# Kernel optimization log

Hardware: AMD Instinct MI355X
Metric: run time of the kernel (lower is better)

The kernel has to match this reference:

```python
import jax, jax.numpy as jnp
import numpy as np

HID = 128          # hidden_dim
IN_DIM = 256       # input_dim
BOT = 128          # bottleneck_dim
OUT = 4            # output_dim
NQ = 131072        # num query (mesh) points
E = 262144         # num grid->query edges
SEQ = 262144       # grid points (64^3)
B = 1
PE_DIM = 4 * HID   # 512, sincos embed dim over ndim=4


def _linear_params(key, fin, fout):
    k1, k2 = jax.random.split(key)
    lim = 1.0 / np.sqrt(fin)
    w = jax.random.uniform(k1, (fin, fout), minval=-lim, maxval=lim, dtype=jnp.float32)
    b = jax.random.uniform(k2, (fout,), minval=-lim, maxval=lim, dtype=jnp.float32)
    return w, b


def setup_inputs() -> dict:
    key = jax.random.key(0)
    ks = jax.random.split(key, 10)
    x = jax.random.normal(ks[0], (B, SEQ, IN_DIM), dtype=jnp.float32)
    # raw positions in [0, 200) so query_pos/100 - 1 lands in [-1, 1)
    query_pos = jax.random.uniform(ks[1], (NQ, 3), dtype=jnp.float32) * 200.0
    qidx = jnp.sort(jax.random.randint(ks[2], (E,), 0, NQ))          # sorted, as segment_csr assumes
    gidx = jax.random.randint(ks[3], (E,), 0, B * SEQ)
    grid_to_query_edges = jnp.stack([qidx, gidx], axis=1)            # [E, 2] (query_idx, grid_idx)

    msg_w0, msg_b0 = _linear_params(ks[4], IN_DIM + PE_DIM, 512)
    msg_w1, msg_b1 = _linear_params(ks[5], 512, 256)
    msg_w2, msg_b2 = _linear_params(ks[6], 256, BOT)
    pred_w0, pred_b0 = _linear_params(ks[7], BOT, 256)
    pred_w1, pred_b1 = _linear_params(ks[8], 256, OUT)
    return dict(x=x, query_pos=query_pos, grid_to_query_edges=grid_to_query_edges,
                msg_w0=msg_w0, msg_b0=msg_b0, msg_w1=msg_w1, msg_b1=msg_b1,
                msg_w2=msg_w2, msg_b2=msg_b2,
                pred_w0=pred_w0, pred_b0=pred_b0, pred_w1=pred_w1, pred_b1=pred_b1)


def _sincos_embed(coords):
    # coords: [N, 4]; dim=512 -> 128 per coord -> 64 frequencies (no padding needed)
    eff = PE_DIM // 4
    omega = 1.0 / (10000.0 ** (jnp.arange(0, eff, 2, dtype=jnp.float32) / eff))  # [64]
    out = coords[..., None] * omega                                  # [N, 4, 64]
    emb = jnp.concatenate([jnp.sin(out), jnp.cos(out)], axis=-1)     # [N, 4, 128]
    return emb.reshape(coords.shape[0], -1)                          # [N, 512]


def _gelu(x):
    return jax.nn.gelu(x, approximate=False)  # torch nn.GELU default is exact erf


def reference(x, query_pos, grid_to_query_edges,
              msg_w0, msg_b0, msg_w1, msg_b1, msg_w2, msg_b2,
              pred_w0, pred_b0, pred_w1, pred_b1):
    qp = query_pos / 100.0 - 1.0
    ones = jnp.ones((qp.shape[0], 1), dtype=qp.dtype)
    qp = jnp.concatenate([qp, ones], axis=1)                         # [NQ, 4]
    pe = _sincos_embed(qp)                                           # [NQ, 512]

    xf = x.reshape(-1, x.shape[-1])                                  # [B*SEQ, IN_DIM]
    qidx = grid_to_query_edges[:, 0]
    gidx = grid_to_query_edges[:, 1]

    feat = jnp.concatenate([xf[gidx], pe[qidx]], axis=1)             # [E, 768]
    h = _gelu(feat @ msg_w0 + msg_b0)
    h = _gelu(h @ msg_w1 + msg_b1)
    h = h @ msg_w2 + msg_b2                                          # [E, BOT]

    nq = qp.shape[0]
    sums = jax.ops.segment_sum(h, qidx, num_segments=nq)             # [NQ, BOT]
    counts = jax.ops.segment_sum(jnp.ones((h.shape[0],), h.dtype), qidx, num_segments=nq)
    mean = sums / jnp.maximum(counts, 1.0)[:, None]                  # empty segments -> 0 (segment_csr mean)

    out = _gelu(mean @ pred_w0 + pred_b0) @ pred_w1 + pred_b1        # [NQ, OUT]
    return out
```

## Files before the change

kernel.cpp:

```cpp
#include <hip/hip_runtime.h>
#include <cmath>

#define IN_DIM   256
#define H0_DIM   512
#define H1_DIM   256
#define BOT      128
#define NQ_      131072
#define NE_      262144
#define SEQ_     262144
#define QWIN     32768
#define NWIN     (NQ_/QWIN)
#define PE_K     384

static const size_t OFF_XH    = 0;
static const size_t OFF_XL    = 134217728;
static const size_t OFF_Z     = 268435456;
static const size_t OFF_PEH   = 536870912;
static const size_t OFF_PEL   = 562036736;
static const size_t OFF_H2    = 738197504;
static const size_t OFF_W0AH  = 872415232;
static const size_t OFF_W0AL  = 872677376;
static const size_t OFF_W0BH  = 872939520;
static const size_t OFF_W0BL  = 873332736;
static const size_t OFF_W1H   = 873725952;
static const size_t OFF_W1L   = 873988096;
static const size_t OFF_W2H   = 874250240;
static const size_t OFF_W2L   = 874315776;
static const size_t OFF_PW0H  = 874381312;
static const size_t OFF_PW0L  = 874446848;
static const size_t OFF_BCONST= 874512384;
static const size_t OFF_START = 874514432;
static const size_t OFF_MEANH = 0;
static const size_t OFF_MEANL = 33554432;
static const size_t OFF_G1    = 268435456;

typedef __attribute__((ext_vector_type(8))) short bf16x8;
typedef __attribute__((ext_vector_type(4))) float f32x4;

__device__ __forceinline__ float gelu_f(float v) {
    return v * 0.5f * (1.0f + erff(v * 0.7071067811865476f));
}
__device__ __forceinline__ unsigned short f2bf(float f) {
    unsigned int u = __float_as_uint(f);
    unsigned int r = (u + 0x7FFFu + ((u >> 16) & 1u)) >> 16;
    return (unsigned short)r;
}
__device__ __forceinline__ float bf2f(unsigned short h) {
    return __uint_as_float(((unsigned int)h) << 16);
}
__device__ __forceinline__ unsigned int pack2(unsigned short a, unsigned short b) {
    return (unsigned int)a | ((unsigned int)b << 16);
}
__device__ __forceinline__ void stage16(const void* g, void* l) {
    __builtin_amdgcn_global_load_lds(
        (const __attribute__((address_space(1))) unsigned int*)g,
        (__attribute__((address_space(3))) unsigned int*)l,
        16, 0, 0);
}
__device__ __forceinline__ void cvt4(const float4 v, unsigned int* hw, unsigned int* lw) {
    const unsigned short a = f2bf(v.x), b = f2bf(v.y), c = f2bf(v.z), d = f2bf(v.w);
    hw[0] = pack2(a, b); hw[1] = pack2(c, d);
    lw[0] = pack2(f2bf(v.x - bf2f(a)), f2bf(v.y - bf2f(b)));
    lw[1] = pack2(f2bf(v.z - bf2f(c)), f2bf(v.w - bf2f(d)));
}

__global__ __launch_bounds__(256) void conv_x(
    const float* __restrict__ x,
    unsigned short* __restrict__ xH, unsigned short* __restrict__ xL)
{
    const int wv = threadIdx.x >> 6;
    const int l  = threadIdx.x & 63;
    const int row = blockIdx.x * 4 + wv;
    const size_t base = (size_t)row * IN_DIM + l * 4;
    float4 v = *(const float4*)&x[base];
    unsigned short h0 = f2bf(v.x), h1 = f2bf(v.y), h2 = f2bf(v.z), h3 = f2bf(v.w);
    uint2 H, L;
    H.x = pack2(h0, h1); H.y = pack2(h2, h3);
    L.x = pack2(f2bf(v.x - bf2f(h0)), f2bf(v.y - bf2f(h1)));
    L.y = pack2(f2bf(v.z - bf2f(h2)), f2bf(v.w - bf2f(h3)));
    *(uint2*)&xH[base] = H;
    *(uint2*)&xL[base] = L;
}

__global__ __launch_bounds__(256) void conv_w(
    const float* __restrict__ W, unsigned short* __restrict__ WTh,
    unsigned short* __restrict__ WTl, int K, int N)
{
    int idx = blockIdx.x * 256 + threadIdx.x;
    if (idx >= K * N) return;
    int k = idx / N, n = idx % N;
    float v = W[idx];
    unsigned short h = f2bf(v);
    WTh[(size_t)n * K + k] = h;
    WTl[(size_t)n * K + k] = f2bf(v - bf2f(h));
}

__global__ __launch_bounds__(256) void bias_fold(
    const float* __restrict__ w0, const float* __restrict__ b0,
    float* __restrict__ bconst)
{
    int n = blockIdx.x * 256 + threadIdx.x;
    if (n >= H0_DIM) return;
    float s = b0[n];
    for (int j = 0; j < 64; ++j) {
        float om = exp2f((float)j * (-13.287712379549449f / 64.0f));
        s += sinf(om) * w0[(size_t)(640 + j) * H0_DIM + n];
        s += cosf(om) * w0[(size_t)(704 + j) * H0_DIM + n];
    }
    bconst[n] = s;
}

__global__ __launch_bounds__(256) void seg_offsets(
    const int* __restrict__ edges, int* __restrict__ start)
{
    int e = blockIdx.x * 256 + threadIdx.x;
    if (e > NE_) return;
    int qc = (e < NE_) ? edges[2 * e] : NQ_;
    int qp = (e > 0) ? edges[2 * e - 2] : -1;
    for (int q = qp + 1; q <= qc; ++q) start[q] = e;
}

__global__ __launch_bounds__(256) void build_pe(
    const float* __restrict__ qpos, int qbase,
    unsigned short* __restrict__ peH, unsigned short* __restrict__ peL)
{
    const int wv = threadIdx.x >> 6;
    const int l  = threadIdx.x & 63;
    const int i  = blockIdx.x * 4 + wv;
    const int i0 = l * 8;
    if (i0 >= PE_K) return;
    const int q  = qbase + i;
    const size_t base = (size_t)i * PE_K;

    const int cc = i0 >> 7;
    const int j0 = i0 & 127;
    const float cv = qpos[q * 3 + cc] * 0.01f - 1.0f;
    const bool is_sin = (j0 < 64);
    const int jj0 = j0 & 63;
    unsigned int hw[4], lw[4];
    #pragma unroll
    for (int p2 = 0; p2 < 4; ++p2) {
        unsigned short hh[2], ll[2];
        #pragma unroll
        for (int s = 0; s < 2; ++s) {
            int jj = jj0 + p2 * 2 + s;
            float om  = exp2f((float)jj * (-13.287712379549449f / 64.0f));
            float arg = cv * om;
            float v   = is_sin ? __sinf(arg) : __cosf(arg);
            unsigned short h = f2bf(v);
            hh[s] = h; ll[s] = f2bf(v - bf2f(h));
        }
        hw[p2] = pack2(hh[0], hh[1]);
        lw[p2] = pack2(ll[0], ll[1]);
    }
    uint4 H, L;
    H.x = hw[0]; H.y = hw[1]; H.z = hw[2]; H.w = hw[3];
    L.x = lw[0]; L.y = lw[1]; L.z = lw[2]; L.w = lw[3];
    *(uint4*)&peH[base + i0] = H;
    *(uint4*)&peL[base + i0] = L;
}

template <int ACT, int OUT_MODE, int GATHER>
__global__ __launch_bounds__(256) void gemm_mfma(
    const unsigned short* __restrict__ Ah, const unsigned short* __restrict__ Al,
    const unsigned short* __restrict__ Bh, const unsigned short* __restrict__ Bl,
    const float* __restrict__ bias,
    float* __restrict__ Cf, unsigned short* __restrict__ ChO, unsigned short* __restrict__ ClO,
    int M, int K, int N,
    const int* __restrict__ gp, const float* __restrict__ Zw)
{
    __shared__ __align__(16) short lds[4][128][32];

    const int tid = threadIdx.x;
    const int w   = tid >> 6;
    const int l   = tid & 63;
    const int l16 = l & 15;
    const int lq  = l >> 4;
    const int bm  = blockIdx.y * 128;
    const int bn  = blockIdx.x * 128;
    const int wm  = (w & 1) * 64;
    const int wn  = (w >> 1) * 64;

    f32x4 acc[4][4];
    #pragma unroll
    for (int i = 0; i < 4; ++i)
        #pragma unroll
        for (int j = 0; j < 4; ++j)
            acc[i][j] = (f32x4){0.f, 0.f, 0.f, 0.f};

    const int jrow = l >> 2;
    const int jkc  = l & 3;
    const int t0 = w * 2, t1 = t0 + 1;
    const int r0 = t0 * 16 + jrow, r1 = t1 * 16 + jrow;

    size_t arow0, arow1;
    if (GATHER) {
        arow0 = (size_t)gp[2 * (bm + r0) + 1] * K;
        arow1 = (size_t)gp[2 * (bm + r1) + 1] * K;
    } else {
        arow0 = (size_t)(bm + r0) * K;
        arow1 = (size_t)(bm + r1) * K;
    }
    const size_t brow0 = (size_t)(bn + r0) * K;
    const size_t brow1 = (size_t)(bn + r1) * K;
    short* d00 = &lds[0][0][0] + t0 * 512;
    short* d01 = &lds[1][0][0] + t0 * 512;
    short* d02 = &lds[2][0][0] + t0 * 512;
    short* d03 = &lds[3][0][0] + t0 * 512;
    short* d10 = &lds[0][0][0] + t1 * 512;
    short* d11 = &lds[1][0][0] + t1 * 512;
    short* d12 = &lds[2][0][0] + t1 * 512;
    short* d13 = &lds[3][0][0] + t1 * 512;

    for (int k0 = 0; k0 < K; k0 += 32) {
        const int ko = k0 + jkc * 8;
        stage16(Ah + arow0 + ko, d00);
        stage16(Al + arow0 + ko, d01);
        stage16(Bh + brow0 + ko, d02);
        stage16(Bl + brow0 + ko, d03);
        stage16(Ah + arow1 + ko, d10);
        stage16(Al + arow1 + ko, d11);
        stage16(Bh + brow1 + ko, d12);
        stage16(Bl + brow1 + ko, d13);
        __syncthreads();

        bf16x8 ah[4], al[4], bh[4], bl[4];
        #pragma unroll
        for (int i = 0; i < 4; ++i) {
            ah[i] = *(const bf16x8*)&lds[0][wm + i*16 + l16][lq*8];
            al[i] = *(const bf16x8*)&lds[1][wm + i*16 + l16][lq*8];
            bh[i] = *(const bf16x8*)&lds[2][wn + i*16 + l16][lq*8];
            bl[i] = *(const bf16x8*)&lds[3][wn + i*16 + l16][lq*8];
        }
        #pragma unroll
        for (int i = 0; i < 4; ++i)
            #pragma unroll
            for (int j = 0; j < 4; ++j) {
                acc[i][j] = __builtin_amdgcn_mfma_f32_16x16x32_bf16(ah[i], bh[j], acc[i][j], 0, 0, 0);
                acc[i][j] = __builtin_amdgcn_mfma_f32_16x16x32_bf16(ah[i], bl[j], acc[i][j], 0, 0, 0);
                acc[i][j] = __builtin_amdgcn_mfma_f32_16x16x32_bf16(al[i], bh[j], acc[i][j], 0, 0, 0);
            }
        __syncthreads();
    }

    if (OUT_MODE == 0) {
        #pragma unroll
        for (int j = 0; j < 4; ++j) {
            int n = bn + wn + j * 16 + l16;
            float bv = bias[n];
            #pragma unroll
            for (int i = 0; i < 4; ++i) {
                int mrow = bm + wm + i * 16 + lq * 4;
                #pragma unroll
                for (int r = 0; r < 4; ++r) {
                    float v = acc[i][j][r] + bv;
                    if (ACT) v = gelu_f(v);
                    Cf[(size_t)(mrow + r) * N + n] = v;
                }
            }
        }
    } else if (OUT_MODE == 1) {
        float* lbuf = ((float*)&lds[0][0][0]) + w * 2048;
        #pragma unroll
        for (int h = 0; h < 2; ++h) {
            #pragma unroll
            for (int j2 = 0; j2 < 2; ++j2) {
                int j = 2 * h + j2;
                float bv = bias[bn + wn + j * 16 + l16];
                #pragma unroll
                for (int i = 0; i < 4; ++i) {
                    #pragma unroll
                    for (int r = 0; r < 4; ++r) {
                        int rowq = i * 16 + lq * 4 + r;
                        int col  = j2 * 16 + l16;
                        float v = acc[i][j][r] + bv;
                        if (ACT) v = gelu_f(v);
                        lbuf[rowq * 32 + (((col >> 2) ^ (rowq & 7)) << 2) + (col & 3)] = v;
                    }
                }
            }
            __syncthreads();
            {
                const size_t grow = (size_t)(bm + wm + l);
                unsigned short* ph = ChO + grow * N + bn + wn + h * 32;
                unsigned short* pl = ClO + grow * N + bn + wn + h * 32;
                #pragma unroll
                for (int cc = 0; cc < 4; ++cc) {
                    unsigned int hw[4], lw[4];
                    #pragma unroll
                    for (int c2 = 0; c2 < 2; ++c2) {
                        int cq = cc * 2 + c2;
                        float4 v = *(const float4*)&lbuf[l * 32 + ((cq ^ (l & 7)) << 2)];
                        unsigned short ha = f2bf(v.x), hb = f2bf(v.y);
                        unsigned short hc = f2bf(v.z), hd = f2bf(v.w);
                        hw[c2*2+0] = pack2(ha, hb);
                        hw[c2*2+1] = pack2(hc, hd);
                        lw[c2*2+0] = pack2(f2bf(v.x - bf2f(ha)), f2bf(v.y - bf2f(hb)));
                        lw[c2*2+1] = pack2(f2bf(v.z - bf2f(hc)), f2bf(v.w - bf2f(hd)));
                    }
                    uint4 H, L;
                    H.x = hw[0]; H.y = hw[1]; H.z = hw[2]; H.w = hw[3];
                    L.x = lw[0]; L.y = lw[1]; L.z = lw[2]; L.w = lw[3];
                    *(uint4*)&ph[cc * 8] = H;
                    *(uint4*)&pl[cc * 8] = L;
                }
            }
            __syncthreads();
        }
    } else {
        const int q = gp[2 * (bm + wm + l)];
        float* lbuf = ((float*)&lds[0][0][0]) + w * 2048;
        #pragma unroll
        for (int h = 0; h < 2; ++h) {
            #pragma unroll
            for (int j2 = 0; j2 < 2; ++j2) {
                int j = 2 * h + j2;
                #pragma unroll
                for (int i = 0; i < 4; ++i) {
                    #pragma unroll
                    for (int r = 0; r < 4; ++r) {
                        int rowq = i * 16 + lq * 4 + r;
                        int col  = j2 * 16 + l16;
                        lbuf[rowq * 32 + (((col >> 2) ^ (rowq & 7)) << 2) + (col & 3)] = acc[i][j][r];
                    }
                }
            }
            __syncthreads();
            {
                const size_t grow = (size_t)(bm + wm + l);
                const float* zrow = Zw + (size_t)q * H0_DIM + bn + wn + h * 32;
                unsigned short* ph = ChO + grow * N + bn + wn + h * 32;
                unsigned short* pl = ClO + grow * N + bn + wn + h * 32;
                #pragma unroll
                for (int cc = 0; cc < 4; ++cc) {
                    unsigned int hw[4], lw[4];
                    #pragma unroll
                    for (int c2 = 0; c2 < 2; ++c2) {
                        int cq = cc * 2 + c2;
                        float4 v = *(const float4*)&lbuf[l * 32 + ((cq ^ (l & 7)) << 2)];
                        float4 z = *(const float4*)&zrow[cq * 4];
                        v.x = gelu_f(v.x + z.x); v.y = gelu_f(v.y + z.y);
                        v.z = gelu_f(v.z + z.z); v.w = gelu_f(v.w + z.w);
                        unsigned short ha = f2bf(v.x), hb = f2bf(v.y);
                        unsigned short hc = f2bf(v.z), hd = f2bf(v.w);
                        hw[c2*2+0] = pack2(ha, hb);
                        hw[c2*2+1] = pack2(hc, hd);
                        lw[c2*2+0] = pack2(f2bf(v.x - bf2f(ha)), f2bf(v.y - bf2f(hb)));
                        lw[c2*2+1] = pack2(f2bf(v.z - bf2f(hc)), f2bf(v.w - bf2f(hd)));
                    }
                    uint4 H, L;
                    H.x = hw[0]; H.y = hw[1]; H.z = hw[2]; H.w = hw[3];
                    L.x = lw[0]; L.y = lw[1]; L.z = lw[2]; L.w = lw[3];
                    *(uint4*)&ph[cc * 8] = H;
                    *(uint4*)&pl[cc * 8] = L;
                }
            }
            __syncthreads();
        }
    }
}

__global__ __launch_bounds__(512, 2) void fused_edge(
    const unsigned short* __restrict__ xHg, const unsigned short* __restrict__ xLg,
    const unsigned short* __restrict__ w0aHg, const unsigned short* __restrict__ w0aLg,
    const unsigned short* __restrict__ w1Hg, const unsigned short* __restrict__ w1Lg,
    const unsigned short* __restrict__ w2Hg, const unsigned short* __restrict__ w2Lg,
    const float* __restrict__ Zg, const float* __restrict__ b1g,
    const float* __restrict__ b2g, const int* __restrict__ gp,
    float* __restrict__ h2g)
{
    extern __shared__ __align__(16) short smem[];
    short* stg = smem;
    short* h0h = smem + 16384;
    short* h0l = smem + 32768;

    const int tid = threadIdx.x;
    const int w   = tid >> 6;
    const int l   = tid & 63;
    const int l16 = l & 15;
    const int lq  = l >> 4;
    const int bm  = blockIdx.x * 128;

    const int wm  = (w & 1) * 64;
    const int wn  = (w >> 1) * 32;
    const int wn1 = (w >> 1) * 64;

    const int srow  = l >> 2;
    const int sunit = l & 3;
    const int r_s   = w * 16 + srow;
    const size_t a_off = (size_t)gp[2 * (bm + r_s) + 1] * IN_DIM + sunit * 8;
    const int q_e = gp[2 * (bm + wm + l)];
    float* lbuf = ((float*)smem) + w * 1024;

    f32x4 h1acc[4][4];
    #pragma unroll
    for (int i = 0; i < 4; ++i)
        #pragma unroll
        for (int j = 0; j < 4; ++j)
            h1acc[i][j] = (f32x4){0.f, 0.f, 0.f, 0.f};

    for (int c = 0; c < 4; ++c) {
        const size_t b0_off = (size_t)(c * 128 + r_s) * IN_DIM + sunit * 8;
        f32x4 acc1[4][2];
        #pragma unroll
        for (int i = 0; i < 4; ++i)
            #pragma unroll
            for (int j = 0; j < 2; ++j)
                acc1[i][j] = (f32x4){0.f, 0.f, 0.f, 0.f};

        stage16(xHg + a_off,    stg + w * 512);
        stage16(xLg + a_off,    stg + 4096 + w * 512);
        stage16(w0aHg + b0_off, stg + 8192 + w * 512);
        stage16(w0aLg + b0_off, stg + 12288 + w * 512);
        __syncthreads();
        for (int ks = 0; ks < 8; ++ks) {
            bf16x8 ah[4], al[4], bh[2], bl[2];
            #pragma unroll
            for (int i = 0; i < 4; ++i) {
                const int ro = (wm + i * 16 + l16) * 32 + lq * 8;
                ah[i] = *(const bf16x8*)&stg[ro];
                al[i] = *(const bf16x8*)&stg[4096 + ro];
            }
            #pragma unroll
            for (int j = 0; j < 2; ++j) {
                const int ro = (wn + j * 16 + l16) * 32 + lq * 8;
                bh[j] = *(const bf16x8*)&stg[8192 + ro];
                bl[j] = *(const bf16x8*)&stg[12288 + ro];
            }
            __syncthreads();
            if (ks < 7) {
                const int k0n = (ks + 1) * 32;
                stage16(xHg + a_off + k0n,    stg + w * 512);
                stage16(xLg + a_off + k0n,    stg + 4096 + w * 512);
                stage16(w0aHg + b0_off + k0n, stg + 8192 + w * 512);
                stage16(w0aLg + b0_off + k0n, stg + 12288 + w * 512);
            }
            #pragma unroll
            for (int i = 0; i < 4; ++i)
                #pragma unroll
                for (int j = 0; j < 2; ++j) {
                    acc1[i][j] = __builtin_amdgcn_mfma_f32_16x16x32_bf16(ah[i], bh[j], acc1[i][j], 0, 0, 0);
                    acc1[i][j] = __builtin_amdgcn_mfma_f32_16x16x32_bf16(ah[i], bl[j], acc1[i][j], 0, 0, 0);
                    acc1[i][j] = __builtin_amdgcn_mfma_f32_16x16x32_bf16(al[i], bh[j], acc1[i][j], 0, 0, 0);
                }
            __syncthreads();
        }

        #pragma unroll
        for (int hh = 0; hh < 2; ++hh) {
            #pragma unroll
            for (int i = 0; i < 4; ++i)
                #pragma unroll
                for (int r = 0; r < 4; ++r) {
                    const int rowq = i * 16 + lq * 4 + r;
                    lbuf[rowq * 16 + ((((l16 >> 2) ^ (rowq & 3)) << 2) | (l16 & 3))] = acc1[i][hh][r];
                }
            __syncthreads();
            {
                const int row = wm + l;
                const float* zrow = Zg + (size_t)q_e * H0_DIM + c * 128 + wn + hh * 16;
                unsigned int hw[8], lw[8];
                #pragma unroll
                for (int cq = 0; cq < 4; ++cq) {
                    float4 v = *(const float4*)&lbuf[l * 16 + ((cq ^ (l & 3)) << 2)];
                    const float4 z = *(const float4*)&zrow[cq * 4];
                    v.x = gelu_f(v.x + z.x); v.y = gelu_f(v.y + z.y);
                    v.z = gelu_f(v.z + z.z); v.w = gelu_f(v.w + z.w);
                    cvt4(v, &hw[cq * 2], &lw[cq * 2]);
                }
                const int u0 = (wn + hh * 16) >> 3;
                const int o0 = row * 128 + (((u0    ) ^ (row & 7)) << 3);
                const int o1 = row * 128 + (((u0 + 1) ^ (row & 7)) << 3);
                uint4 H0, H1, L0, L1;
                H0.x = hw[0]; H0.y = hw[1]; H0.z = hw[2]; H0.w = hw[3];
                H1.x = hw[4]; H1.y = hw[5]; H1.z = hw[6]; H1.w = hw[7];
                L0.x = lw[0]; L0.y = lw[1]; L0.z = lw[2]; L0.w = lw[3];
                L1.x = lw[4]; L1.y = lw[5]; L1.z = lw[6]; L1.w = lw[7];
                *(uint4*)&h0h[o0] = H0; *(uint4*)&h0h[o1] = H1;
                *(uint4*)&h0l[o0] = L0; *(uint4*)&h0l[o1] = L1;
            }
            __syncthreads();
        }

        {
            const size_t r0 = (size_t)(w * 32 + srow) * H0_DIM + c * 128 + sunit * 8;
            stage16(w1Hg + r0,               stg + w * 1024);
            stage16(w1Hg + r0 + 16 * H0_DIM, stg + w * 1024 + 512);
            stage16(w1Lg + r0,               stg + 8192 + w * 1024);
            stage16(w1Lg + r0 + 16 * H0_DIM, stg + 8192 + w * 1024 + 512);
        }
        __syncthreads();
        for (int ks = 0; ks < 4; ++ks) {
            bf16x8 ah[4], al[4], bh[4], bl[4];
            #pragma unroll
            for (int i = 0; i < 4; ++i) {
                const int row = wm + i * 16 + l16;
                const int uo = (((ks * 4 + lq) ^ (row & 7)) << 3);
                ah[i] = *(const bf16x8*)&h0h[row * 128 + uo];
                al[i] = *(const bf16x8*)&h0l[row * 128 + uo];
            }
            #pragma unroll
            for (int j = 0; j < 4; ++j) {
                const int ro = (wn1 + j * 16 + l16) * 32 + lq * 8;
                bh[j] = *(const bf16x8*)&stg[ro];
                bl[j] = *(const bf16x8*)&stg[8192 + ro];
            }
            __syncthreads();
            if (ks < 3) {
                const size_t r0 = (size_t)(w * 32 + srow) * H0_DIM + c * 128 + (ks + 1) * 32 + sunit * 8;
                stage16(w1Hg + r0,               stg + w * 1024);
                stage16(w1Hg + r0 + 16 * H0_DIM, stg + w * 1024 + 512);
                stage16(w1Lg + r0,               stg + 8192 + w * 1024);
                stage16(w1Lg + r0 + 16 * H0_DIM, stg + 8192 + w * 1024 + 512);
            }
            #pragma unroll
            for (int i = 0; i < 4; ++i)
                #pragma unroll
                for (int j = 0; j < 4; ++j) {
                    h1acc[i][j] = __builtin_amdgcn_mfma_f32_16x16x32_bf16(ah[i], bh[j], h1acc[i][j], 0, 0, 0);
                    h1acc[i][j] = __builtin_amdgcn_mfma_f32_16x16x32_bf16(ah[i], bl[j], h1acc[i][j], 0, 0, 0);
                    h1acc[i][j] = __builtin_amdgcn_mfma_f32_16x16x32_bf16(al[i], bh[j], h1acc[i][j], 0, 0, 0);
                }
            __syncthreads();
        }
    }

    f32x4 acc2[4][2];
    #pragma unroll
    for (int i = 0; i < 4; ++i)
        #pragma unroll
        for (int j = 0; j < 2; ++j)
            acc2[i][j] = (f32x4){0.f, 0.f, 0.f, 0.f};
    const int mykh = w >> 2;

    for (int kh = 0; kh < 2; ++kh) {
        #pragma unroll
        for (int hh = 0; hh < 4; ++hh) {
            if (mykh == kh) {
                const float bv = b1g[wn1 + hh * 16 + l16];
                #pragma unroll
                for (int i = 0; i < 4; ++i)
                    #pragma unroll
                    for (int r = 0; r < 4; ++r) {
                        const int rowq = i * 16 + lq * 4 + r;
                        lbuf[rowq * 16 + ((((l16 >> 2) ^ (rowq & 3)) << 2) | (l16 & 3))] =
                            gelu_f(h1acc[i][hh][r] + bv);
                    }
            }
            __syncthreads();
            if (mykh == kh) {
                const int row = wm + l;
                unsigned int hw[8], lw[8];
                #pragma unroll
                for (int cq = 0; cq < 4; ++cq) {
                    float4 v = *(const float4*)&lbuf[l * 16 + ((cq ^ (l & 3)) << 2)];
                    cvt4(v, &hw[cq * 2], &lw[cq * 2]);
                }
                const int u0 = ((wn1 & 127) + hh * 16) >> 3;
                const int o0 = row * 128 + (((u0    ) ^ (row & 7)) << 3);
                const int o1 = row * 128 + (((u0 + 1) ^ (row & 7)) << 3);
                uint4 H0, H1, L0, L1;
                H0.x = hw[0]; H0.y = hw[1]; H0.z = hw[2]; H0.w = hw[3];
                H1.x = hw[4]; H1.y = hw[5]; H1.z = hw[6]; H1.w = hw[7];
                L0.x = lw[0]; L0.y = lw[1]; L0.z = lw[2]; L0.w = lw[3];
                L1.x = lw[4]; L1.y = lw[5]; L1.z = lw[6]; L1.w = lw[7];
                *(uint4*)&h0h[o0] = H0; *(uint4*)&h0h[o1] = H1;
                *(uint4*)&h0l[o0] = L0; *(uint4*)&h0l[o1] = L1;
            }
            __syncthreads();
        }

        {
            const unsigned short* Wsrc = (w < 4) ? w2Hg : w2Lg;
            const size_t r0 = (size_t)((w & 3) * 32 + srow) * H1_DIM + kh * 128 + sunit * 8;
            short* dst = stg + (w >> 2) * 4096 + (w & 3) * 1024;
            stage16(Wsrc + r0,               dst);
            stage16(Wsrc + r0 + 16 * H1_DIM, dst + 512);
        }
        __syncthreads();
        for (int ks = 0; ks < 4; ++ks) {
            bf16x8 ah[4], al[4], bh[2], bl[2];
            #pragma unroll
            for (int i = 0; i < 4; ++i) {
                const int row = wm + i * 16 + l16;
                const int uo = (((ks * 4 + lq) ^ (row & 7)) << 3);
                ah[i] = *(const bf16x8*)&h0h[row * 128 + uo];
                al[i] = *(const bf16x8*)&h0l[row * 128 + uo];
            }
            #pragma unroll
            for (int j = 0; j < 2; ++j) {
                const int ro = (wn + j * 16 + l16) * 32 + lq * 8;
                bh[j] = *(const bf16x8*)&stg[ro];
                bl[j] = *(const bf16x8*)&stg[4096 + ro];
            }
            __syncthreads();
            if (ks < 3) {
                const unsigned short* Wsrc = (w < 4) ? w2Hg : w2Lg;
                const size_t r0 = (size_t)((w & 3) * 32 + srow) * H1_DIM + kh * 128 + (ks + 1) * 32 + sunit * 8;
                short* dst = stg + (w >> 2) * 4096 + (w & 3) * 1024;
                stage16(Wsrc + r0,               dst);
                stage16(Wsrc + r0 + 16 * H1_DIM, dst + 512);
            }
            #pragma unroll
            for (int i = 0; i < 4; ++i)
                #pragma unroll
                for (int j = 0; j < 2; ++j) {
                    acc2[i][j] = __builtin_amdgcn_mfma_f32_16x16x32_bf16(ah[i], bh[j], acc2[i][j], 0, 0, 0);
                    acc2[i][j] = __builtin_amdgcn_mfma_f32_16x16x32_bf16(ah[i], bl[j], acc2[i][j], 0, 0, 0);
                    acc2[i][j] = __builtin_amdgcn_mfma_f32_16x16x32_bf16(al[i], bh[j], acc2[i][j], 0, 0, 0);
                }
            __syncthreads();
        }
    }

    #pragma unroll
    for (int j = 0; j < 2; ++j) {
        const int n = wn + j * 16 + l16;
        const float bv = b2g[n];
        #pragma unroll
        for (int i = 0; i < 4; ++i) {
            const int er = bm + wm + i * 16 + lq * 4;
            #pragma unroll
            for (int r = 0; r < 4; ++r)
                h2g[(size_t)(er + r) * BOT + n] = acc2[i][j][r] + bv;
        }
    }
}

__global__ __launch_bounds__(256) void seg_mean(
    const int* __restrict__ start, const float* __restrict__ h2,
    unsigned short* __restrict__ mH, unsigned short* __restrict__ mL)
{
    const int t = threadIdx.x;
    const int q = blockIdx.x * 8 + (t >> 5);
    const int quad = t & 31;
    const int s = start[q];
    const int e = start[q + 1];

    float4 acc = make_float4(0.f, 0.f, 0.f, 0.f);
    for (int i = s; i < e; ++i) {
        const float4 v = *(const float4*)&h2[(size_t)i * BOT + quad * 4];
        acc.x += v.x; acc.y += v.y; acc.z += v.z; acc.w += v.w;
    }
    const float inv = 1.0f / (float)((e - s) > 0 ? (e - s) : 1);
    float m0 = acc.x * inv, m1 = acc.y * inv, m2 = acc.z * inv, m3 = acc.w * inv;
    unsigned short h0 = f2bf(m0), h1 = f2bf(m1), h2s = f2bf(m2), h3 = f2bf(m3);
    uint2 H, L;
    H.x = pack2(h0, h1); H.y = pack2(h2s, h3);
    L.x = pack2(f2bf(m0 - bf2f(h0)), f2bf(m1 - bf2f(h1)));
    L.y = pack2(f2bf(m2 - bf2f(h2s)), f2bf(m3 - bf2f(h3)));
    *(uint2*)&mH[(size_t)q * BOT + quad * 4] = H;
    *(uint2*)&mL[(size_t)q * BOT + quad * 4] = L;
}

__global__ __launch_bounds__(256) void pred1_kernel(
    const float* __restrict__ g1, const float* __restrict__ w,
    const float* __restrict__ b, float* __restrict__ out)
{
    const int wave = threadIdx.x >> 6;
    const int lane = threadIdx.x & 63;
    const int row  = blockIdx.x * 4 + wave;

    const float* g = g1 + (size_t)row * 256;
    float a0 = 0, a1 = 0, a2 = 0, a3 = 0;
    #pragma unroll
    for (int i = 0; i < 4; ++i) {
        int k = lane + 64 * i;
        float gv = g[k];
        const float* wr = w + k * 4;
        a0 = fmaf(gv, wr[0], a0);
        a1 = fmaf(gv, wr[1], a1);
        a2 = fmaf(gv, wr[2], a2);
        a3 = fmaf(gv, wr[3], a3);
    }
    #pragma unroll
    for (int off = 32; off > 0; off >>= 1) {
        a0 += __shfl_down(a0, off, 64);
        a1 += __shfl_down(a1, off, 64);
        a2 += __shfl_down(a2, off, 64);
        a3 += __shfl_down(a3, off, 64);
    }
    if (lane == 0) {
        float4 o = {a0 + b[0], a1 + b[1], a2 + b[2], a3 + b[3]};
        *(float4*)&out[(size_t)row * 4] = o;
    }
}

extern "C" void kernel_launch(void* const* d_in, const int* in_sizes, int n_in,
                              void* d_out, int out_size, void* d_ws, size_t ws_size,
                              hipStream_t stream)
{
    const float* x    = (const float*)d_in[0];
    const float* qpos = (const float*)d_in[1];
    const int*   edges= (const int*)  d_in[2];
    const float* w0   = (const float*)d_in[3];
    const float* b0   = (const float*)d_in[4];
    const float* w1   = (const float*)d_in[5];
    const float* b1   = (const float*)d_in[6];
    const float* w2   = (const float*)d_in[7];
    const float* b2   = (const float*)d_in[8];
    const float* pw0  = (const float*)d_in[9];
    const float* pb0  = (const float*)d_in[10];
    const float* pw1  = (const float*)d_in[11];
    const float* pb1  = (const float*)d_in[12];
    float* out = (float*)d_out;

    char* ws = (char*)d_ws;
    unsigned short* xH    = (unsigned short*)(ws + OFF_XH);
    unsigned short* xL    = (unsigned short*)(ws + OFF_XL);
    float*          Z     = (float*)(ws + OFF_Z);
    unsigned short* peH   = (unsigned short*)(ws + OFF_PEH);
    unsigned short* peL   = (unsigned short*)(ws + OFF_PEL);
    float*          h2    = (float*)(ws + OFF_H2);
    unsigned short* w0aH  = (unsigned short*)(ws + OFF_W0AH);
    unsigned short* w0aL  = (unsigned short*)(ws + OFF_W0AL);
    unsigned short* w0bH  = (unsigned short*)(ws + OFF_W0BH);
    unsigned short* w0bL  = (unsigned short*)(ws + OFF_W0BL);
    unsigned short* w1H   = (unsigned short*)(ws + OFF_W1H);
    unsigned short* w1L   = (unsigned short*)(ws + OFF_W1L);
    unsigned short* w2H   = (unsigned short*)(ws + OFF_W2H);
    unsigned short* w2L   = (unsigned short*)(ws + OFF_W2L);
    unsigned short* pw0H  = (unsigned short*)(ws + OFF_PW0H);
    unsigned short* pw0L  = (unsigned short*)(ws + OFF_PW0L);
    float*          bconst= (float*)(ws + OFF_BCONST);
    int*            start = (int*)(ws + OFF_START);
    unsigned short* meanH = (unsigned short*)(ws + OFF_MEANH);
    unsigned short* meanL = (unsigned short*)(ws + OFF_MEANL);
    float*          g1    = (float*)(ws + OFF_G1);

    static bool attr_done = false;
    if (!attr_done) {
        hipFuncSetAttribute(reinterpret_cast<const void*>(&fused_edge),
                            hipFuncAttributeMaxDynamicSharedMemorySize, 98304);
        attr_done = true;
    }

    conv_x<<<SEQ_/4, 256, 0, stream>>>(x, xH, xL);
    conv_w<<<(IN_DIM*H0_DIM + 255)/256, 256, 0, stream>>>(w0, w0aH, w0aL, IN_DIM, H0_DIM);
    conv_w<<<(PE_K*H0_DIM + 255)/256, 256, 0, stream>>>(w0 + (size_t)IN_DIM*H0_DIM, w0bH, w0bL, PE_K, H0_DIM);
    conv_w<<<(H0_DIM*H1_DIM + 255)/256, 256, 0, stream>>>(w1, w1H, w1L, H0_DIM, H1_DIM);
    conv_w<<<(H1_DIM*BOT + 255)/256, 256, 0, stream>>>(w2, w2H, w2L, H1_DIM, BOT);
    conv_w<<<(BOT*H1_DIM + 255)/256, 256, 0, stream>>>(pw0, pw0H, pw0L, BOT, H1_DIM);
    bias_fold<<<2, 256, 0, stream>>>(w0, b0, bconst);
    seg_offsets<<<(NE_ + 1 + 255)/256, 256, 0, stream>>>(edges, start);

    for (int wn = 0; wn < NWIN; ++wn) {
        build_pe<<<QWIN/4, 256, 0, stream>>>(qpos, wn * QWIN, peH, peL);
        gemm_mfma<0, 0, 0><<<dim3(H0_DIM/128, QWIN/128), 256, 0, stream>>>(
            peH, peL, w0bH, w0bL, bconst, Z + (size_t)wn * QWIN * H0_DIM,
            nullptr, nullptr, QWIN, PE_K, H0_DIM, nullptr, nullptr);
    }

    fused_edge<<<NE_/128, 512, 98304, stream>>>(
        xH, xL, w0aH, w0aL, w1H, w1L, w2H, w2L,
        Z, b1, b2, edges, h2);

    seg_mean<<<NQ_/8, 256, 0, stream>>>(start, h2, meanH, meanL);
    gemm_mfma<1, 0, 0><<<dim3(H1_DIM/128, NQ_/128), 256, 0, stream>>>(
        meanH, meanL, pw0H, pw0L, pb0, g1, nullptr, nullptr,
        NQ_, BOT, H1_DIM, nullptr, nullptr);
    pred1_kernel<<<NQ_/4, 256, 0, stream>>>(g1, pw1, pb1, out);
}
```

Before: 1.672 ms.

## Shrink fused edge kernel tile to 64 edges with 4 warps

The fused edge MLP kernel now processes 64 edges per block with 256 threads instead of 128 edges with 512 threads. Every warp covers all 64 rows and takes a distinct column slice, so all staging, epilogue and LDS layouts are rewritten and dynamic shared memory drops from 96KB to 64KB. The aim is higher occupancy and more blocks in flight, paying for it with more weight staging per edge, since each weight tile is now reused across only 64 rows. The unused OUT_MODE 1/2 epilogues of the generic GEMM are also deleted.

```diff
diff --git a/kernel.cpp b/kernel.cpp
--- a/kernel.cpp
+++ b/kernel.cpp
@@ -259,108 +259,10 @@
                 }
             }
         }
-    } else if (OUT_MODE == 1) {
-        float* lbuf = ((float*)&lds[0][0][0]) + w * 2048;
-        #pragma unroll
-        for (int h = 0; h < 2; ++h) {
-            #pragma unroll
-            for (int j2 = 0; j2 < 2; ++j2) {
-                int j = 2 * h + j2;
-                float bv = bias[bn + wn + j * 16 + l16];
-                #pragma unroll
-                for (int i = 0; i < 4; ++i) {
-                    #pragma unroll
-                    for (int r = 0; r < 4; ++r) {
-                        int rowq = i * 16 + lq * 4 + r;
-                        int col  = j2 * 16 + l16;
-                        float v = acc[i][j][r] + bv;
-                        if (ACT) v = gelu_f(v);
-                        lbuf[rowq * 32 + (((col >> 2) ^ (rowq & 7)) << 2) + (col & 3)] = v;
-                    }
-                }
-            }
-            __syncthreads();
-            {
-                const size_t grow = (size_t)(bm + wm + l);
-                unsigned short* ph = ChO + grow * N + bn + wn + h * 32;
-                unsigned short* pl = ClO + grow * N + bn + wn + h * 32;
-                #pragma unroll
-                for (int cc = 0; cc < 4; ++cc) {
-                    unsigned int hw[4], lw[4];
-                    #pragma unroll
-                    for (int c2 = 0; c2 < 2; ++c2) {
-                        int cq = cc * 2 + c2;
-                        float4 v = *(const float4*)&lbuf[l * 32 + ((cq ^ (l & 7)) << 2)];
-                        unsigned short ha = f2bf(v.x), hb = f2bf(v.y);
-                        unsigned short hc = f2bf(v.z), hd = f2bf(v.w);
-                        hw[c2*2+0] = pack2(ha, hb);
-                        hw[c2*2+1] = pack2(hc, hd);
-                        lw[c2*2+0] = pack2(f2bf(v.x - bf2f(ha)), f2bf(v.y - bf2f(hb)));
-                        lw[c2*2+1] = pack2(f2bf(v.z - bf2f(hc)), f2bf(v.w - bf2f(hd)));
-                    }
-                    uint4 H, L;
-                    H.x = hw[0]; H.y = hw[1]; H.z = hw[2]; H.w = hw[3];
-                    L.x = lw[0]; L.y = lw[1]; L.z = lw[2]; L.w = lw[3];
-                    *(uint4*)&ph[cc * 8] = H;
-                    *(uint4*)&pl[cc * 8] = L;
-                }
-            }
-            __syncthreads();
-        }
-    } else {
-        const int q = gp[2 * (bm + wm + l)];
-        float* lbuf = ((float*)&lds[0][0][0]) + w * 2048;
-        #pragma unroll
-        for (int h = 0; h < 2; ++h) {
-            #pragma unroll
-            for (int j2 = 0; j2 < 2; ++j2) {
-                int j = 2 * h + j2;
-                #pragma unroll
-                for (int i = 0; i < 4; ++i) {
-                    #pragma unroll
-                    for (int r = 0; r < 4; ++r) {
-                        int rowq = i * 16 + lq * 4 + r;
-                        int col  = j2 * 16 + l16;
-                        lbuf[rowq * 32 + (((col >> 2) ^ (rowq & 7)) << 2) + (col & 3)] = acc[i][j][r];
-                    }
-                }
-            }
-            __syncthreads();
-            {
-                const size_t grow = (size_t)(bm + wm + l);
-                const float* zrow = Zw + (size_t)q * H0_DIM + bn + wn + h * 32;
-                unsigned short* ph = ChO + grow * N + bn + wn + h * 32;
-                unsigned short* pl = ClO + grow * N + bn + wn + h * 32;
-                #pragma unroll
-                for (int cc = 0; cc < 4; ++cc) {
-                    unsigned int hw[4], lw[4];
-                    #pragma unroll
-                    for (int c2 = 0; c2 < 2; ++c2) {
-                        int cq = cc * 2 + c2;
-                        float4 v = *(const float4*)&lbuf[l * 32 + ((cq ^ (l & 7)) << 2)];
-                        float4 z = *(const float4*)&zrow[cq * 4];
-                        v.x = gelu_f(v.x + z.x); v.y = gelu_f(v.y + z.y);
-                        v.z = gelu_f(v.z + z.z); v.w = gelu_f(v.w + z.w);
-                        unsigned short ha = f2bf(v.x), hb = f2bf(v.y);
-                        unsigned short hc = f2bf(v.z), hd = f2bf(v.w);
-                        hw[c2*2+0] = pack2(ha, hb);
-                        hw[c2*2+1] = pack2(hc, hd);
-                        lw[c2*2+0] = pack2(f2bf(v.x - bf2f(ha)), f2bf(v.y - bf2f(hb)));
-                        lw[c2*2+1] = pack2(f2bf(v.z - bf2f(hc)), f2bf(v.w - bf2f(hd)));
-                    }
-                    uint4 H, L;
-                    H.x = hw[0]; H.y = hw[1]; H.z = hw[2]; H.w = hw[3];
-                    L.x = lw[0]; L.y = lw[1]; L.z = lw[2]; L.w = lw[3];
-                    *(uint4*)&ph[cc * 8] = H;
-                    *(uint4*)&pl[cc * 8] = L;
-                }
-            }
-            __syncthreads();
-        }
-    }
-}
-
-__global__ __launch_bounds__(512, 2) void fused_edge(
+    }
+}
+
+__global__ __launch_bounds__(256, 2) void fused_edge(
     const unsigned short* __restrict__ xHg, const unsigned short* __restrict__ xLg,
     const unsigned short* __restrict__ w0aHg, const unsigned short* __restrict__ w0aLg,
     const unsigned short* __restrict__ w1Hg, const unsigned short* __restrict__ w1Lg,
@@ -372,25 +274,32 @@
     extern __shared__ __align__(16) short smem[];
     short* stg = smem;
     short* h0h = smem + 16384;
-    short* h0l = smem + 32768;
+    short* h0l = smem + 24576;
 
     const int tid = threadIdx.x;
     const int w   = tid >> 6;
     const int l   = tid & 63;
     const int l16 = l & 15;
     const int lq  = l >> 4;
-    const int bm  = blockIdx.x * 128;
-
-    const int wm  = (w & 1) * 64;
-    const int wn  = (w >> 1) * 32;
-    const int wn1 = (w >> 1) * 64;
-
-    const int srow  = l >> 2;
-    const int sunit = l & 3;
-    const int r_s   = w * 16 + srow;
-    const size_t a_off = (size_t)gp[2 * (bm + r_s) + 1] * IN_DIM + sunit * 8;
-    const int q_e = gp[2 * (bm + wm + l)];
-    float* lbuf = ((float*)smem) + w * 1024;
+    const int bm  = blockIdx.x * 64;
+
+    const int wn_p = w * 32;
+    const int wn1  = w * 64;
+
+    const int rx = tid >> 2;
+    const int ux = tid & 3;
+    const size_t xoff = (size_t)gp[2 * (bm + rx) + 1] * IN_DIM + ux * 8;
+    const int q_e = gp[2 * (bm + l)];
+    float* lbuf = ((float*)stg) + w * 2048;
+
+    short* stgAh  = stg;
+    short* stgAl  = stg + 2048;
+    short* stgBh  = stg + 4096;
+    short* stgBl  = stg + 8192;
+    short* stgW1h = stg;
+    short* stgW1l = stg + 8192;
+    short* stgW2h = stg;
+    short* stgW2l = stg + 4096;
 
     f32x4 h1acc[4][4];
     #pragma unroll
@@ -400,7 +309,6 @@
             h1acc[i][j] = (f32x4){0.f, 0.f, 0.f, 0.f};
 
     for (int c = 0; c < 4; ++c) {
-        const size_t b0_off = (size_t)(c * 128 + r_s) * IN_DIM + sunit * 8;
         f32x4 acc1[4][2];
         #pragma unroll
         for (int i = 0; i < 4; ++i)
@@ -408,32 +316,40 @@
             for (int j = 0; j < 2; ++j)
                 acc1[i][j] = (f32x4){0.f, 0.f, 0.f, 0.f};
 
-        stage16(xHg + a_off,    stg + w * 512);
-        stage16(xLg + a_off,    stg + 4096 + w * 512);
-        stage16(w0aHg + b0_off, stg + 8192 + w * 512);
-        stage16(w0aLg + b0_off, stg + 12288 + w * 512);
+        {
+            const size_t wo = (size_t)(c * 128 + rx) * IN_DIM + ux * 8;
+            stage16(xHg + xoff, stgAh + tid * 8);
+            stage16(xLg + xoff, stgAl + tid * 8);
+            stage16(w0aHg + wo,                      stgBh + tid * 8);
+            stage16(w0aLg + wo,                      stgBl + tid * 8);
+            stage16(w0aHg + wo + (size_t)64 * IN_DIM, stgBh + 2048 + tid * 8);
+            stage16(w0aLg + wo + (size_t)64 * IN_DIM, stgBl + 2048 + tid * 8);
+        }
         __syncthreads();
         for (int ks = 0; ks < 8; ++ks) {
             bf16x8 ah[4], al[4], bh[2], bl[2];
             #pragma unroll
             for (int i = 0; i < 4; ++i) {
-                const int ro = (wm + i * 16 + l16) * 32 + lq * 8;
-                ah[i] = *(const bf16x8*)&stg[ro];
-                al[i] = *(const bf16x8*)&stg[4096 + ro];
+                const int ro = (i * 16 + l16) * 32 + lq * 8;
+                ah[i] = *(const bf16x8*)&stgAh[ro];
+                al[i] = *(const bf16x8*)&stgAl[ro];
             }
             #pragma unroll
             for (int j = 0; j < 2; ++j) {
-                const int ro = (wn + j * 16 + l16) * 32 + lq * 8;
-                bh[j] = *(const bf16x8*)&stg[8192 + ro];
-                bl[j] = *(const bf16x8*)&stg[12288 + ro];
+                const int ro = (wn_p + j * 16 + l16) * 32 + lq * 8;
+                bh[j] = *(const bf16x8*)&stgBh[ro];
+                bl[j] = *(const bf16x8*)&stgBl[ro];
             }
             __syncthreads();
             if (ks < 7) {
-                const int k0n = (ks + 1) * 32;
-                stage16(xHg + a_off + k0n,    stg + w * 512);
-                stage16(xLg + a_off + k0n,    stg + 4096 + w * 512);
-                stage16(w0aHg + b0_off + k0n, stg + 8192 + w * 512);
-                stage16(w0aLg + b0_off + k0n, stg + 12288 + w * 512);
+                const int ko = (ks + 1) * 32;
+                const size_t wo = (size_t)(c * 128 + rx) * IN_DIM + ko + ux * 8;
+                stage16(xHg + xoff + ko, stgAh + tid * 8);
+                stage16(xLg + xoff + ko, stgAl + tid * 8);
+                stage16(w0aHg + wo,                      stgBh + tid * 8);
+                stage16(w0aLg + wo,                      stgBl + tid * 8);
+                stage16(w0aHg + wo + (size_t)64 * IN_DIM, stgBh + 2048 + tid * 8);
+                stage16(w0aLg + wo + (size_t)64 * IN_DIM, stgBl + 2048 + tid * 8);
             }
             #pragma unroll
             for (int i = 0; i < 4; ++i)
@@ -447,30 +363,33 @@
         }
 
         #pragma unroll
-        for (int hh = 0; hh < 2; ++hh) {
+        for (int j = 0; j < 2; ++j)
             #pragma unroll
             for (int i = 0; i < 4; ++i)
                 #pragma unroll
                 for (int r = 0; r < 4; ++r) {
                     const int rowq = i * 16 + lq * 4 + r;
-                    lbuf[rowq * 16 + ((((l16 >> 2) ^ (rowq & 3)) << 2) | (l16 & 3))] = acc1[i][hh][r];
-                }
-            __syncthreads();
-            {
-                const int row = wm + l;
-                const float* zrow = Zg + (size_t)q_e * H0_DIM + c * 128 + wn + hh * 16;
+                    const int u = j * 4 + (l16 >> 2);
+                    lbuf[rowq * 32 + (((u ^ (rowq & 7)) << 2) | (l16 & 3))] = acc1[i][j][r];
+                }
+        __syncthreads();
+        {
+            const float* zrow = Zg + (size_t)q_e * H0_DIM + c * 128 + wn_p;
+            #pragma unroll
+            for (int g = 0; g < 2; ++g) {
                 unsigned int hw[8], lw[8];
                 #pragma unroll
-                for (int cq = 0; cq < 4; ++cq) {
-                    float4 v = *(const float4*)&lbuf[l * 16 + ((cq ^ (l & 3)) << 2)];
+                for (int c2 = 0; c2 < 4; ++c2) {
+                    const int cq = g * 4 + c2;
+                    float4 v = *(const float4*)&lbuf[l * 32 + ((cq ^ (l & 7)) << 2)];
                     const float4 z = *(const float4*)&zrow[cq * 4];
                     v.x = gelu_f(v.x + z.x); v.y = gelu_f(v.y + z.y);
                     v.z = gelu_f(v.z + z.z); v.w = gelu_f(v.w + z.w);
-                    cvt4(v, &hw[cq * 2], &lw[cq * 2]);
-                }
-                const int u0 = (wn + hh * 16) >> 3;
-                const int o0 = row * 128 + (((u0    ) ^ (row & 7)) << 3);
-                const int o1 = row * 128 + (((u0 + 1) ^ (row & 7)) << 3);
+                    cvt4(v, &hw[c2 * 2], &lw[c2 * 2]);
+                }
+                const int u0 = (wn_p >> 3) + g * 2;
+                const int o0 = l * 128 + (((u0    ) ^ (l & 7)) << 3);
+                const int o1 = l * 128 + (((u0 + 1) ^ (l & 7)) << 3);
                 uint4 H0, H1, L0, L1;
                 H0.x = hw[0]; H0.y = hw[1]; H0.z = hw[2]; H0.w = hw[3];
                 H1.x = hw[4]; H1.y = hw[5]; H1.z = hw[6]; H1.w = hw[7];
@@ -479,39 +398,41 @@
                 *(uint4*)&h0h[o0] = H0; *(uint4*)&h0h[o1] = H1;
                 *(uint4*)&h0l[o0] = L0; *(uint4*)&h0l[o1] = L1;
             }
-            __syncthreads();
-        }
+        }
+        __syncthreads();
 
         {
-            const size_t r0 = (size_t)(w * 32 + srow) * H0_DIM + c * 128 + sunit * 8;
-            stage16(w1Hg + r0,               stg + w * 1024);
-            stage16(w1Hg + r0 + 16 * H0_DIM, stg + w * 1024 + 512);
-            stage16(w1Lg + r0,               stg + 8192 + w * 1024);
-            stage16(w1Lg + r0 + 16 * H0_DIM, stg + 8192 + w * 1024 + 512);
+            #pragma unroll
+            for (int p = 0; p < 4; ++p) {
+                const size_t o = (size_t)(rx + 64 * p) * H0_DIM + c * 128 + ux * 8;
+                stage16(w1Hg + o, stgW1h + p * 2048 + tid * 8);
+                stage16(w1Lg + o, stgW1l + p * 2048 + tid * 8);
+            }
         }
         __syncthreads();
         for (int ks = 0; ks < 4; ++ks) {
             bf16x8 ah[4], al[4], bh[4], bl[4];
             #pragma unroll
             for (int i = 0; i < 4; ++i) {
-                const int row = wm + i * 16 + l16;
-                const int uo = (((ks * 4 + lq) ^ (row & 7)) << 3);
+                const int row = i * 16 + l16;
+                const int uo = ((ks * 4 + lq) ^ (row & 7)) << 3;
                 ah[i] = *(const bf16x8*)&h0h[row * 128 + uo];
                 al[i] = *(const bf16x8*)&h0l[row * 128 + uo];
             }
             #pragma unroll
             for (int j = 0; j < 4; ++j) {
                 const int ro = (wn1 + j * 16 + l16) * 32 + lq * 8;
-                bh[j] = *(const bf16x8*)&stg[ro];
-                bl[j] = *(const bf16x8*)&stg[8192 + ro];
+                bh[j] = *(const bf16x8*)&stgW1h[ro];
+                bl[j] = *(const bf16x8*)&stgW1l[ro];
             }
             __syncthreads();
             if (ks < 3) {
-                const size_t r0 = (size_t)(w * 32 + srow) * H0_DIM + c * 128 + (ks + 1) * 32 + sunit * 8;
-                stage16(w1Hg + r0,               stg + w * 1024);
-                stage16(w1Hg + r0 + 16 * H0_DIM, stg + w * 1024 + 512);
-                stage16(w1Lg + r0,               stg + 8192 + w * 1024);
-                stage16(w1Lg + r0 + 16 * H0_DIM, stg + 8192 + w * 1024 + 512);
+                #pragma unroll
+                for (int p = 0; p < 4; ++p) {
+                    const size_t o = (size_t)(rx + 64 * p) * H0_DIM + c * 128 + (ks + 1) * 32 + ux * 8;
+                    stage16(w1Hg + o, stgW1h + p * 2048 + tid * 8);
+                    stage16(w1Lg + o, stgW1l + p * 2048 + tid * 8);
+                }
             }
             #pragma unroll
             for (int i = 0; i < 4; ++i)
@@ -531,75 +452,86 @@
         #pragma unroll
         for (int j = 0; j < 2; ++j)
             acc2[i][j] = (f32x4){0.f, 0.f, 0.f, 0.f};
-    const int mykh = w >> 2;
 
     for (int kh = 0; kh < 2; ++kh) {
-        #pragma unroll
-        for (int hh = 0; hh < 4; ++hh) {
-            if (mykh == kh) {
-                const float bv = b1g[wn1 + hh * 16 + l16];
-                #pragma unroll
-                for (int i = 0; i < 4; ++i)
+        const bool my = ((w >> 1) == kh);
+        #pragma unroll
+        for (int j2 = 0; j2 < 2; ++j2) {
+            if (my) {
+                #pragma unroll
+                for (int jj = 0; jj < 2; ++jj) {
+                    const int j = j2 * 2 + jj;
+                    const float bv = b1g[wn1 + j * 16 + l16];
                     #pragma unroll
-                    for (int r = 0; r < 4; ++r) {
-                        const int rowq = i * 16 + lq * 4 + r;
-                        lbuf[rowq * 16 + ((((l16 >> 2) ^ (rowq & 3)) << 2) | (l16 & 3))] =
-                            gelu_f(h1acc[i][hh][r] + bv);
+                    for (int i = 0; i < 4; ++i)
+                        #pragma unroll
+                        for (int r = 0; r < 4; ++r) {
+                            const int rowq = i * 16 + lq * 4 + r;
+                            const int u = jj * 4 + (l16 >> 2);
+                            lbuf[rowq * 32 + (((u ^ (rowq & 7)) << 2) | (l16 & 3))] =
+                                gelu_f(h1acc[i][j][r] + bv);
+                        }
+                }
+            }
+            __syncthreads();
+            if (my) {
+                const int colb = (w & 1) * 64 + j2 * 32;
+                #pragma unroll
+                for (int g = 0; g < 2; ++g) {
+                    unsigned int hw[8], lw[8];
+                    #pragma unroll
+                    for (int c2 = 0; c2 < 4; ++c2) {
+                        const int cq = g * 4 + c2;
+                        float4 v = *(const float4*)&lbuf[l * 32 + ((cq ^ (l & 7)) << 2)];
+                        cvt4(v, &hw[c2 * 2], &lw[c2 * 2]);
                     }
-            }
-            __syncthreads();
-            if (mykh == kh) {
-                const int row = wm + l;
-                unsigned int hw[8], lw[8];
-                #pragma unroll
-                for (int cq = 0; cq < 4; ++cq) {
-                    float4 v = *(const float4*)&lbuf[l * 16 + ((cq ^ (l & 3)) << 2)];
-                    cvt4(v, &hw[cq * 2], &lw[cq * 2]);
-                }
-                const int u0 = ((wn1 & 127) + hh * 16) >> 3;
-                const int o0 = row * 128 + (((u0    ) ^ (row & 7)) << 3);
-                const int o1 = row * 128 + (((u0 + 1) ^ (row & 7)) << 3);
-                uint4 H0, H1, L0, L1;
-                H0.x = hw[0]; H0.y = hw[1]; H0.z = hw[2]; H0.w = hw[3];
-                H1.x = hw[4]; H1.y = hw[5]; H1.z = hw[6]; H1.w = hw[7];
-                L0.x = lw[0]; L0.y = lw[1]; L0.z = lw[2]; L0.w = lw[3];
-                L1.x = lw[4]; L1.y = lw[5]; L1.z = lw[6]; L1.w = lw[7];
-                *(uint4*)&h0h[o0] = H0; *(uint4*)&h0h[o1] = H1;
-                *(uint4*)&h0l[o0] = L0; *(uint4*)&h0l[o1] = L1;
+                    const int u0 = ((colb + g * 16) >> 3);
+                    const int o0 = l * 128 + (((u0    ) ^ (l & 7)) << 3);
+                    const int o1 = l * 128 + (((u0 + 1) ^ (l & 7)) << 3);
+                    uint4 H0, H1, L0, L1;
+                    H0.x = hw[0]; H0.y = hw[1]; H0.z = hw[2]; H0.w = hw[3];
+                    H1.x = hw[4]; H1.y = hw[5]; H1.z = hw[6]; H1.w = hw[7];
+                    L0.x = lw[0]; L0.y = lw[1]; L0.z = lw[2]; L0.w = lw[3];
+                    L1.x = lw[4]; L1.y = lw[5]; L1.z = lw[6]; L1.w = lw[7];
+                    *(uint4*)&h0h[o0] = H0; *(uint4*)&h0h[o1] = H1;
+                    *(uint4*)&h0l[o0] = L0; *(uint4*)&h0l[o1] = L1;
+                }
             }
             __syncthreads();
         }
 
         {
-            const unsigned short* Wsrc = (w < 4) ? w2Hg : w2Lg;
-            const size_t r0 = (size_t)((w & 3) * 32 + srow) * H1_DIM + kh * 128 + sunit * 8;
-            short* dst = stg + (w >> 2) * 4096 + (w & 3) * 1024;
-            stage16(Wsrc + r0,               dst);
-            stage16(Wsrc + r0 + 16 * H1_DIM, dst + 512);
+            #pragma unroll
+            for (int p = 0; p < 2; ++p) {
+                const size_t o = (size_t)(rx + 64 * p) * H1_DIM + kh * 128 + ux * 8;
+                stage16(w2Hg + o, stgW2h + p * 2048 + tid * 8);
+                stage16(w2Lg + o, stgW2l + p * 2048 + tid * 8);
+            }
         }
         __syncthreads();
         for (int ks = 0; ks < 4; ++ks) {
             bf16x8 ah[4], al[4], bh[2], bl[2];
             #pragma unroll
             for (int i = 0; i < 4; ++i) {
-                const int row = wm + i * 16 + l16;
-                const int uo = (((ks * 4 + lq) ^ (row & 7)) << 3);
+                const int row = i * 16 + l16;
+                const int uo = ((ks * 4 + lq) ^ (row & 7)) << 3;
                 ah[i] = *(const bf16x8*)&h0h[row * 128 + uo];
                 al[i] = *(const bf16x8*)&h0l[row * 128 + uo];
             }
             #pragma unroll
             for (int j = 0; j < 2; ++j) {
-                const int ro = (wn + j * 16 + l16) * 32 + lq * 8;
-                bh[j] = *(const bf16x8*)&stg[ro];
-                bl[j] = *(const bf16x8*)&stg[4096 + ro];
+                const int ro = (wn_p + j * 16 + l16) * 32 + lq * 8;
+                bh[j] = *(const bf16x8*)&stgW2h[ro];
+                bl[j] = *(const bf16x8*)&stgW2l[ro];
             }
             __syncthreads();
             if (ks < 3) {
-                const unsigned short* Wsrc = (w < 4) ? w2Hg : w2Lg;
-                const size_t r0 = (size_t)((w & 3) * 32 + srow) * H1_DIM + kh * 128 + (ks + 1) * 32 + sunit * 8;
-                short* dst = stg + (w >> 2) * 4096 + (w & 3) * 1024;
-                stage16(Wsrc + r0,               dst);
-                stage16(Wsrc + r0 + 16 * H1_DIM, dst + 512);
+                #pragma unroll
+                for (int p = 0; p < 2; ++p) {
+                    const size_t o = (size_t)(rx + 64 * p) * H1_DIM + kh * 128 + (ks + 1) * 32 + ux * 8;
+                    stage16(w2Hg + o, stgW2h + p * 2048 + tid * 8);
+                    stage16(w2Lg + o, stgW2l + p * 2048 + tid * 8);
+                }
             }
             #pragma unroll
             for (int i = 0; i < 4; ++i)
@@ -615,11 +547,11 @@
 
     #pragma unroll
     for (int j = 0; j < 2; ++j) {
-        const int n = wn + j * 16 + l16;
+        const int n = wn_p + j * 16 + l16;
         const float bv = b2g[n];
         #pragma unroll
         for (int i = 0; i < 4; ++i) {
-            const int er = bm + wm + i * 16 + lq * 4;
+            const int er = bm + i * 16 + lq * 4;
             #pragma unroll
             for (int r = 0; r < 4; ++r)
                 h2g[(size_t)(er + r) * BOT + n] = acc2[i][j][r] + bv;
@@ -731,7 +663,7 @@
     static bool attr_done = false;
     if (!attr_done) {
         hipFuncSetAttribute(reinterpret_cast<const void*>(&fused_edge),
-                            hipFuncAttributeMaxDynamicSharedMemorySize, 98304);
+                            hipFuncAttributeMaxDynamicSharedMemorySize, 65536);
         attr_done = true;
     }
 
@@ -751,7 +683,7 @@
             nullptr, nullptr, QWIN, PE_K, H0_DIM, nullptr, nullptr);
     }
 
-    fused_edge<<<NE_/128, 512, 98304, stream>>>(
+    fused_edge<<<NE_/64, 256, 65536, stream>>>(
         xH, xL, w0aH, w0aL, w1H, w1L, w2H, w2L,
         Z, b1, b2, edges, h2);
 
```

Result: faster. 1.580 ms (-5.5%).
